# Performance work log

Measured on AMD Instinct MI355X. Metric: run time of the kernel, lower is better.

The kernel has to match this reference:

```python
import jax, jax.numpy as jnp
import numpy as np

B, T, C = 4, 2048, 1024
NH = 16
HD = C // NH


def setup_inputs() -> dict:
    key = jax.random.key(0)
    ks = jax.random.split(key, 5)
    s = 1.0 / np.sqrt(C)
    return {
        "x": jax.random.normal(ks[0], (B, T, C), dtype=jnp.float32),
        "W_qkv": jax.random.normal(ks[1], (C, 3 * C), dtype=jnp.float32) * s,
        "b_qkv": jnp.zeros((3 * C,), dtype=jnp.float32),
        "W_out": jax.random.normal(ks[2], (C, C), dtype=jnp.float32) * s,
        "b_out": jnp.zeros((C,), dtype=jnp.float32),
    }


def reference(x, W_qkv, b_qkv, W_out, b_out):
    Bx, Tx, Cx = x.shape
    qkv = x @ W_qkv + b_qkv                      # [B,T,3C]
    q, k, v = jnp.split(qkv, 3, axis=2)
    # [B,T,C] -> [B,NH,T,HD]
    q = q.reshape(Bx, Tx, NH, HD).transpose(0, 2, 1, 3)
    k = k.reshape(Bx, Tx, NH, HD).transpose(0, 2, 1, 3)
    v = v.reshape(Bx, Tx, NH, HD).transpose(0, 2, 1, 3)
    scale = 1.0 / np.sqrt(HD).astype(np.float32)
    attn = jnp.einsum('bhqd,bhkd->bhqk', q, k) * scale  # [B,NH,T,T]
    causal = jnp.tril(jnp.ones((Tx, Tx), dtype=bool))
    attn = jnp.where(causal[None, None], attn, jnp.float32(-jnp.inf))
    attn = jax.nn.softmax(attn, axis=-1)
    out = jnp.einsum('bhqk,bhkd->bhqd', attn, v)        # [B,NH,T,HD]
    out = out.transpose(0, 2, 1, 3).reshape(Bx, Tx, Cx)
    y = out @ W_out + b_out
    return (y, k, v)
```

## Files before the change

kernel.cpp:

```cpp
#include <hip/hip_runtime.h>
#include <cstdint>
#include <cstddef>

typedef __bf16 bf16x8 __attribute__((ext_vector_type(8)));
typedef __bf16 bf16x4 __attribute__((ext_vector_type(4)));
typedef float  f32x4  __attribute__((ext_vector_type(4)));

#define MFMA16(a, b, c) __builtin_amdgcn_mfma_f32_16x16x32_bf16((a), (b), (c), 0, 0, 0)

#define GLL16(gsrc, ldst)                                                              \
  __builtin_amdgcn_global_load_lds((__attribute__((address_space(1))) void*)(gsrc),    \
                                   (__attribute__((address_space(3))) void*)(ldst),    \
                                   16, 0, 0)

#define QSCALE 0.1803368801111204f


__global__ __launch_bounds__(256)
void cvt_f32_bf16(const float* __restrict__ in, __bf16* __restrict__ out, int n4)
{
    int i = blockIdx.x * 256 + threadIdx.x;
    if (i < n4) {
        float4 v = ((const float4*)in)[i];
        bf16x4 o;
        o[0] = (__bf16)v.x; o[1] = (__bf16)v.y; o[2] = (__bf16)v.z; o[3] = (__bf16)v.w;
        ((bf16x4*)out)[i] = o;
    }
}

__global__ __launch_bounds__(256)
void transpose_cvt(const float* __restrict__ in, __bf16* __restrict__ out, int K, int N)
{
    __shared__ __bf16 tile[32][33];
    const int n0 = blockIdx.x * 32, k0 = blockIdx.y * 32;
    const int tx = threadIdx.x, ty = threadIdx.y;
    #pragma unroll
    for (int i = 0; i < 4; ++i)
        tile[ty + i * 8][tx] = (__bf16)in[(size_t)(k0 + ty + i * 8) * N + n0 + tx];
    __syncthreads();
    #pragma unroll
    for (int i = 0; i < 4; ++i)
        out[(size_t)(n0 + ty + i * 8) * K + k0 + tx] = tile[tx][ty + i * 8];
}


__global__ __launch_bounds__(256)
void vtrans(const float* __restrict__ vout, __bf16* __restrict__ vwst)
{
    const int bh = blockIdx.y;
    const int t0 = blockIdx.x * 64;
    const int tid = threadIdx.x;

    __shared__ __bf16 VT[64][68];

    const int tr = tid >> 4;
    const int dc = (tid & 15) * 4;

    float4 vals[4];
    #pragma unroll
    for (int i = 0; i < 4; ++i)
        vals[i] = *(const float4*)&vout[((size_t)bh * 2048 + t0 + tr + 16 * i) * 64 + dc];

    #pragma unroll
    for (int j = 0; j < 4; ++j) {
        bf16x4 pk;
        pk[0] = (__bf16)(&vals[0].x)[j];
        pk[1] = (__bf16)(&vals[1].x)[j];
        pk[2] = (__bf16)(&vals[2].x)[j];
        pk[3] = (__bf16)(&vals[3].x)[j];
        *(bf16x4*)&VT[dc + j][4 * tr] = pk;
    }
    __syncthreads();

    #pragma unroll
    for (int k = 0; k < 2; ++k) {
        const int c = tid + 256 * k;
        const int d = c >> 3, off = (c & 7) * 8;
        bf16x8 v = *(const bf16x8*)&VT[d][off];
        *(bf16x8*)&vwst[((size_t)bh * 64 + d) * 2048 + t0 + off] = v;
    }
}


__global__ __launch_bounds__(512, 2)
void gemm_qkv(const __bf16* __restrict__ A, const __bf16* __restrict__ Bt,
              const float* __restrict__ bias,
              __bf16* __restrict__ qws, float* __restrict__ kout, float* __restrict__ vout,
              __bf16* __restrict__ kws)
{
    constexpr int K = 1024;
    const int m0 = blockIdx.y * 256, n0 = blockIdx.x * 192;
    const int tid = threadIdx.x;
    const int wave = tid >> 6, lane = tid & 63;
    const int quad = lane >> 4, lr = lane & 15;
    const int wm = wave & 1, wn = wave >> 1;
    const int wrow = wm * 128, wcol = wn * 48;

    __shared__ __bf16 As[2][2][256][32];
    __shared__ __bf16 Bs[2][2][192][32];

    f32x4 acc[8][3];
    #pragma unroll
    for (int mi = 0; mi < 8; ++mi)
      #pragma unroll
      for (int ni = 0; ni < 3; ++ni)
        #pragma unroll
        for (int c = 0; c < 4; ++c) acc[mi][ni][c] = 0.f;

    const __bf16* gA[4];
    #pragma unroll
    for (int l = 0; l < 4; ++l) {
        const int u = tid + 512 * l;
        const int kc = u >> 10;
        const int row = (u >> 2) & 255;
        const int cg = ((u & 3) ^ ((u >> 3) & 3)) * 8;
        gA[l] = A + (size_t)(m0 + row) * K + kc * 32 + cg;
    }
    const __bf16* gB[3];
    #pragma unroll
    for (int l = 0; l < 3; ++l) {
        const int u = tid + 512 * l;
        const int kc = (u >= 768);
        const int row = (u - kc * 768) >> 2;
        const int cg = ((u & 3) ^ ((u >> 3) & 3)) * 8;
        gB[l] = Bt + (size_t)(n0 + row) * K + kc * 32 + cg;
    }
    char* lA = (char*)As + tid * 16;
    char* lB = (char*)Bs + tid * 16;

    const int sw = (quad ^ ((lr >> 1) & 3)) * 8;

    GLL16(gA[0], lA);
    GLL16(gA[1], lA + 8192);
    GLL16(gA[2], lA + 16384);
    GLL16(gA[3], lA + 24576);
    GLL16(gB[0], lB);
    GLL16(gB[1], lB + 8192);
    GLL16(gB[2], lB + 16384);
    GLL16(gA[0] + 64, lA + 32768);
    GLL16(gA[1] + 64, lA + 40960);
    asm volatile("s_waitcnt vmcnt(2)" ::: "memory");
    asm volatile("s_barrier" ::: "memory");

    bf16x8 bfv[3];

#define PHASE(buf, kc, mh, ...)                                                    \
    do {                                                                           \
        if ((mh) == 0) {                                                           \
            bfv[0] = *(const bf16x8*)&Bs[buf][kc][wcol      + lr][sw];             \
            bfv[1] = *(const bf16x8*)&Bs[buf][kc][wcol + 16 + lr][sw];             \
            bfv[2] = *(const bf16x8*)&Bs[buf][kc][wcol + 32 + lr][sw];             \
        }                                                                          \
        bf16x8 af0 = *(const bf16x8*)&As[buf][kc][wrow + (mh)*64      + lr][sw];   \
        bf16x8 af1 = *(const bf16x8*)&As[buf][kc][wrow + (mh)*64 + 16 + lr][sw];   \
        bf16x8 af2 = *(const bf16x8*)&As[buf][kc][wrow + (mh)*64 + 32 + lr][sw];   \
        bf16x8 af3 = *(const bf16x8*)&As[buf][kc][wrow + (mh)*64 + 48 + lr][sw];   \
        __VA_ARGS__                                                                \
        asm volatile("s_barrier" ::: "memory");                                    \
        __builtin_amdgcn_s_setprio(1);                                             \
        acc[(mh)*4+0][0] = MFMA16(af0, bfv[0], acc[(mh)*4+0][0]);                  \
        acc[(mh)*4+0][1] = MFMA16(af0, bfv[1], acc[(mh)*4+0][1]);                  \
        acc[(mh)*4+0][2] = MFMA16(af0, bfv[2], acc[(mh)*4+0][2]);                  \
        acc[(mh)*4+1][0] = MFMA16(af1, bfv[0], acc[(mh)*4+1][0]);                  \
        acc[(mh)*4+1][1] = MFMA16(af1, bfv[1], acc[(mh)*4+1][1]);                  \
        acc[(mh)*4+1][2] = MFMA16(af1, bfv[2], acc[(mh)*4+1][2]);                  \
        acc[(mh)*4+2][0] = MFMA16(af2, bfv[0], acc[(mh)*4+2][0]);                  \
        acc[(mh)*4+2][1] = MFMA16(af2, bfv[1], acc[(mh)*4+2][1]);                  \
        acc[(mh)*4+2][2] = MFMA16(af2, bfv[2], acc[(mh)*4+2][2]);                  \
        acc[(mh)*4+3][0] = MFMA16(af3, bfv[0], acc[(mh)*4+3][0]);                  \
        acc[(mh)*4+3][1] = MFMA16(af3, bfv[1], acc[(mh)*4+3][1]);                  \
        acc[(mh)*4+3][2] = MFMA16(af3, bfv[2], acc[(mh)*4+3][2]);                  \
        __builtin_amdgcn_s_setprio(0);                                             \
        asm volatile("s_barrier" ::: "memory");                                    \
    } while (0)

    for (int it = 0; it < 8; ++it) {
        const bool more = (it < 7);

        PHASE(0, 0, 0, {
            GLL16(gA[2] + 64, lA + 16384 + 32768);
            GLL16(gA[3] + 64, lA + 24576 + 32768);
            GLL16(gB[0] + 64, lB + 24576);
            GLL16(gB[1] + 64, lB +  8192 + 24576);
            GLL16(gB[2] + 64, lB + 16384 + 24576);
        });
        PHASE(0, 0, 1, {});
        PHASE(0, 1, 0, {
            if (more) { GLL16(gA[0] + 128, lA); GLL16(gA[1] + 128, lA + 8192); }
        });
        PHASE(0, 1, 1, {
            if (more) asm volatile("s_waitcnt vmcnt(2)" ::: "memory");
            else      asm volatile("s_waitcnt vmcnt(0)" ::: "memory");
        });
        PHASE(1, 0, 0, {
            if (more) {
                GLL16(gA[2] + 128, lA + 16384);
                GLL16(gA[3] + 128, lA + 24576);
                GLL16(gB[0] + 128, lB);
                GLL16(gB[1] + 128, lB + 8192);
                GLL16(gB[2] + 128, lB + 16384);
            }
        });
        PHASE(1, 0, 1, {});
        PHASE(1, 1, 0, {
            if (more) { GLL16(gA[0] + 192, lA + 32768); GLL16(gA[1] + 192, lA + 40960); }
        });
        PHASE(1, 1, 1, {
            if (more) asm volatile("s_waitcnt vmcnt(2)" ::: "memory");
            else      asm volatile("s_waitcnt vmcnt(0)" ::: "memory");
        });

        #pragma unroll
        for (int l = 0; l < 4; ++l) gA[l] += 128;
        #pragma unroll
        for (int l = 0; l < 3; ++l) gB[l] += 128;
    }
#undef PHASE

    #pragma unroll
    for (int ni = 0; ni < 3; ++ni) {
        const int gn = n0 + wcol + ni * 16 + lr;
        const float bv = bias[gn];
        const int sec = gn >> 10;
        const int cn = gn & 1023, hh = cn >> 6, dd = cn & 63;
        #pragma unroll
        for (int mi = 0; mi < 8; ++mi) {
            const int gm0 = m0 + wrow + mi * 16 + quad * 4;
            const int b = gm0 >> 11, t0 = gm0 & 2047;
            const size_t tb = ((size_t)b * 16 + hh) * 2048;
            if (sec == 0) {
                #pragma unroll
                for (int r = 0; r < 4; ++r)
                    qws[(tb + t0 + r) * 64 + dd] = (__bf16)((acc[mi][ni][r] + bv) * QSCALE);
            } else if (sec == 1) {
                #pragma unroll
                for (int r = 0; r < 4; ++r) {
                    const float val = acc[mi][ni][r] + bv;
                    kout[(tb + t0 + r) * 64 + dd] = val;
                    kws [(tb + t0 + r) * 64 + dd] = (__bf16)val;
                }
            } else {
                #pragma unroll
                for (int r = 0; r < 4; ++r)
                    vout[(tb + t0 + r) * 64 + dd] = acc[mi][ni][r] + bv;
            }
        }
    }
}


__global__ __launch_bounds__(256)
void gemm_out(const __bf16* __restrict__ A, const __bf16* __restrict__ Bt,
              const float* __restrict__ bias, float* __restrict__ y)
{
    constexpr int K = 1024;
    const int m0 = blockIdx.y * 64, n0 = blockIdx.x * 128;
    const int tid = threadIdx.x;
    const int wave = tid >> 6, lane = tid & 63;
    const int quad = lane >> 4, lr = lane & 15;
    const int wrow = (wave & 1) * 32, wcol = (wave >> 1) * 64;

    __shared__ __bf16 As[64 * 32];
    __shared__ __bf16 Bs[128 * 32];

    f32x4 acc[2][4];
    #pragma unroll
    for (int mi = 0; mi < 2; ++mi)
      #pragma unroll
      for (int ni = 0; ni < 4; ++ni)
        #pragma unroll
        for (int c = 0; c < 4; ++c) acc[mi][ni][c] = 0.f;

    const int ua = tid, u0 = tid, u1 = tid + 256;
    const int cga = ((ua & 3) ^ ((ua >> 3) & 3)) * 8;
    const int cg0 = ((u0 & 3) ^ ((u0 >> 3) & 3)) * 8;
    const int cg1 = ((u1 & 3) ^ ((u1 >> 3) & 3)) * 8;
    const __bf16* ga  = A  + (size_t)(m0 + (ua >> 2)) * K + cga;
    const __bf16* gb0 = Bt + (size_t)(n0 + (u0 >> 2)) * K + cg0;
    const __bf16* gb1 = Bt + (size_t)(n0 + (u1 >> 2)) * K + cg1;
    __bf16* la  = As + ua * 8;
    __bf16* lb0 = Bs + u0 * 8;
    __bf16* lb1 = Bs + u1 * 8;

    const int sw = (quad ^ ((lr >> 1) & 3)) * 8;

    for (int kt = 0; kt < K; kt += 32) {
        __syncthreads();
        GLL16(ga + kt, la);
        GLL16(gb0 + kt, lb0);
        GLL16(gb1 + kt, lb1);
        __syncthreads();
        bf16x8 af[2], bfv[4];
        #pragma unroll
        for (int mi = 0; mi < 2; ++mi)
            af[mi] = *(const bf16x8*)&As[(wrow + mi * 16 + lr) * 32 + sw];
        #pragma unroll
        for (int ni = 0; ni < 4; ++ni)
            bfv[ni] = *(const bf16x8*)&Bs[(wcol + ni * 16 + lr) * 32 + sw];
        #pragma unroll
        for (int mi = 0; mi < 2; ++mi)
          #pragma unroll
          for (int ni = 0; ni < 4; ++ni)
            acc[mi][ni] = MFMA16(af[mi], bfv[ni], acc[mi][ni]);
    }

    #pragma unroll
    for (int ni = 0; ni < 4; ++ni) {
        const int gn = n0 + wcol + ni * 16 + lr;
        const float bv = bias[gn];
        #pragma unroll
        for (int mi = 0; mi < 2; ++mi) {
            #pragma unroll
            for (int r = 0; r < 4; ++r) {
                const int gm = m0 + wrow + mi * 16 + quad * 4 + r;
                y[(size_t)gm * 1024 + gn] = acc[mi][ni][r] + bv;
            }
        }
    }
}


__global__ __launch_bounds__(256, 2)
void attn_fused(const __bf16* __restrict__ qws, const __bf16* __restrict__ kws,
                const __bf16* __restrict__ vwst, __bf16* __restrict__ attnws)
{
    const int bh = blockIdx.x;
    const int tid = threadIdx.x;
    const int wave = tid >> 6, lane = tid & 63;
    const int quad = lane >> 4, lr = lane & 15;

    const int jqp[2] = { (int)blockIdx.y, 15 - (int)blockIdx.y };
    const int ntp[2] = { 2 * (jqp[0] + 1), 2 * (jqp[1] + 1) };
    const int nt0 = ntp[0];
    const int ntot = 34;

    __shared__ __bf16 Ks [3][2][64][32];
    __shared__ __bf16 Vts[3][2][64][32];
    __shared__ __bf16 Ps [4][32][72];

    const int srow = tid >> 2;
    const int scg  = ((tid & 3) ^ ((tid >> 3) & 3)) * 8;
    const __bf16* kb = kws  + ((size_t)bh * 2048 + srow) * 64 + scg;
    const __bf16* vb = vwst + ((size_t)bh * 64 + srow) * 2048 + scg;
    char* lk = (char*)Ks  + tid * 16;
    char* lv = (char*)Vts + tid * 16;

    const int sw = (quad ^ ((lr >> 1) & 3)) * 8;

    bf16x8 ones;
    #pragma unroll
    for (int j = 0; j < 8; ++j) ones[j] = (__bf16)1.0f;

    bf16x8 aq[2][2][2];
    #pragma unroll
    for (int h = 0; h < 2; ++h)
      #pragma unroll
      for (int mi = 0; mi < 2; ++mi) {
        const __bf16* qb = qws + ((size_t)bh * 2048 + jqp[h] * 128 + wave * 32 + mi * 16 + lr) * 64 + quad * 8;
        aq[h][mi][0] = *(const bf16x8*)qb;
        aq[h][mi][1] = *(const bf16x8*)(qb + 32);
      }

#define PREFETCH(j, buf)                                                \
    do {                                                                \
        GLL16(kb + (size_t)(j) * 4096,      lk + (buf) * 8192);         \
        GLL16(kb + (size_t)(j) * 4096 + 32, lk + (buf) * 8192 + 4096);  \
        GLL16(vb + (j) * 64,                lv + (buf) * 8192);         \
        GLL16(vb + (j) * 64 + 32,           lv + (buf) * 8192 + 4096);  \
    } while (0)

    PREFETCH(0, 0);
    PREFETCH(1, 1);

    bf16x4 oreg[2][2][4];

    int pos = 0;
    for (int h = 0; h < 2; ++h) {
        const int jq = jqp[h];
        const int NT = ntp[h];

        f32x4 o_acc[2][4], l_acc[2];
        #pragma unroll
        for (int mi = 0; mi < 2; ++mi) {
            #pragma unroll
            for (int r = 0; r < 4; ++r) l_acc[mi][r] = 0.f;
            #pragma unroll
            for (int n = 0; n < 4; ++n)
                #pragma unroll
                for (int r = 0; r < 4; ++r) o_acc[mi][n][r] = 0.f;
        }

        for (int jt = 0; jt < NT; ++jt, ++pos) {
            const int cur = pos % 3;
            if (pos + 1 < ntot) {
                asm volatile("s_waitcnt vmcnt(4)" ::: "memory");
            } else {
                asm volatile("s_waitcnt vmcnt(0)" ::: "memory");
            }
            asm volatile("s_waitcnt lgkmcnt(0)" ::: "memory");
            asm volatile("s_barrier" ::: "memory");
            if (pos + 2 < ntot) {
                const int p2 = pos + 2;
                const int nj = (p2 < nt0) ? p2 : p2 - nt0;
                PREFETCH(nj, p2 % 3);
            }

            const bool lastTile = (jt == NT - 1);
            if (!(lastTile && wave < 2)) {
                bf16x8 bk[4][2];
                #pragma unroll
                for (int ni = 0; ni < 4; ++ni) {
                    bk[ni][0] = *(const bf16x8*)&Ks[cur][0][ni * 16 + lr][sw];
                    bk[ni][1] = *(const bf16x8*)&Ks[cur][1][ni * 16 + lr][sw];
                }
                f32x4 sacc[2][4];
                #pragma unroll
                for (int mi = 0; mi < 2; ++mi)
                  #pragma unroll
                  for (int ni = 0; ni < 4; ++ni)
                    #pragma unroll
                    for (int c = 0; c < 4; ++c) sacc[mi][ni][c] = -12.f;
                #pragma unroll
                for (int ni = 0; ni < 4; ++ni)
                  #pragma unroll
                  for (int mi = 0; mi < 2; ++mi) {
                    sacc[mi][ni] = MFMA16(aq[h][mi][0], bk[ni][0], sacc[mi][ni]);
                    sacc[mi][ni] = MFMA16(aq[h][mi][1], bk[ni][1], sacc[mi][ni]);
                  }

                const bool needMask = (jt == NT - 2 && wave < 2) || (lastTile && wave >= 2);
                if (needMask) {
                    const int c0 = jt * 64 + lr;
                    #pragma unroll
                    for (int mi = 0; mi < 2; ++mi) {
                        const int t0 = jq * 128 + wave * 32 + mi * 16 + quad * 4;
                        #pragma unroll
                        for (int ni = 0; ni < 4; ++ni)
                          #pragma unroll
                          for (int r = 0; r < 4; ++r)
                            if (c0 + ni * 16 > t0 + r) sacc[mi][ni][r] = -1e30f;
                    }
                }

                #pragma unroll
                for (int mi = 0; mi < 2; ++mi)
                  #pragma unroll
                  for (int r = 0; r < 4; ++r) {
                    bf16x4 pp;
                    #pragma unroll
                    for (int ni = 0; ni < 4; ++ni)
                        pp[ni] = (__bf16)__builtin_amdgcn_exp2f(sacc[mi][ni][r]);
                    *(bf16x4*)&Ps[wave][mi * 16 + quad * 4 + r][4 * lr] = pp;
                  }

                asm volatile("s_waitcnt lgkmcnt(0)" ::: "memory");

                bf16x8 bv[4][2];
                #pragma unroll
                for (int n = 0; n < 4; ++n) {
                    bv[n][0] = *(const bf16x8*)&Vts[cur][0][n * 16 + lr][sw];
                    bv[n][1] = *(const bf16x8*)&Vts[cur][1][n * 16 + lr][sw];
                }
                #pragma unroll
                for (int mi = 0; mi < 2; ++mi) {
                    bf16x8 ap0 = *(const bf16x8*)&Ps[wave][mi * 16 + lr][quad * 8];
                    bf16x8 ap1 = *(const bf16x8*)&Ps[wave][mi * 16 + lr][32 + quad * 8];
                    l_acc[mi] = MFMA16(ap0, ones, l_acc[mi]);
                    l_acc[mi] = MFMA16(ap1, ones, l_acc[mi]);
                    #pragma unroll
                    for (int n = 0; n < 4; ++n) {
                        o_acc[mi][n] = MFMA16(ap0, bv[n][0], o_acc[mi][n]);
                        o_acc[mi][n] = MFMA16(ap1, bv[n][1], o_acc[mi][n]);
                    }
                }
            }
        }

        #pragma unroll
        for (int mi = 0; mi < 2; ++mi)
          #pragma unroll
          for (int r = 0; r < 4; ++r) {
            const float inv = 1.f / l_acc[mi][r];
            #pragma unroll
            for (int n = 0; n < 4; ++n)
                oreg[h][mi][n][r] = (__bf16)(o_acc[mi][n][r] * inv);
          }
    }

    const int b = bh >> 4, h16 = bh & 15;
    #pragma unroll
    for (int h = 0; h < 2; ++h)
      #pragma unroll
      for (int mi = 0; mi < 2; ++mi)
        #pragma unroll
        for (int r = 0; r < 4; ++r) {
            const int t = jqp[h] * 128 + wave * 32 + mi * 16 + quad * 4 + r;
            #pragma unroll
            for (int n = 0; n < 4; ++n)
                attnws[(((size_t)b * 2048 + t) * 16 + h16) * 64 + n * 16 + lr] =
                    oreg[h][mi][n][r];
        }
#undef PREFETCH
}


extern "C" void kernel_launch(void* const* d_in, const int* in_sizes, int n_in,
                              void* d_out, int out_size, void* d_ws, size_t ws_size,
                              hipStream_t stream)
{
    (void)in_sizes; (void)n_in; (void)out_size; (void)ws_size;

    const float* x    = (const float*)d_in[0];
    const float* Wqkv = (const float*)d_in[1];
    const float* bqkv = (const float*)d_in[2];
    const float* Wout = (const float*)d_in[3];
    const float* bout = (const float*)d_in[4];

    float* y    = (float*)d_out;
    float* kout = y + 8388608;
    float* vout = kout + 8388608;

    char* ws = (char*)d_ws;
    __bf16* xb    = (__bf16*)(ws);
    __bf16* wqkvt = (__bf16*)(ws + (16u << 20));
    __bf16* woutt = (__bf16*)(ws + (22u << 20));
    __bf16* qws   = (__bf16*)(ws + (24u << 20));
    __bf16* kws   = (__bf16*)(ws + (40u << 20));
    __bf16* vwst  = (__bf16*)(ws + (56u << 20));
    __bf16* attnw = (__bf16*)(ws + (72u << 20));

    cvt_f32_bf16<<<8192, 256, 0, stream>>>(x, xb, 2097152);
    transpose_cvt<<<dim3(96, 32), dim3(32, 8), 0, stream>>>(Wqkv, wqkvt, 1024, 3072);
    transpose_cvt<<<dim3(32, 32), dim3(32, 8), 0, stream>>>(Wout, woutt, 1024, 1024);
    gemm_qkv<<<dim3(16, 32), 512, 0, stream>>>(xb, wqkvt, bqkv, qws, kout, vout, kws);
    vtrans<<<dim3(32, 64), 256, 0, stream>>>(vout, vwst);
    attn_fused<<<dim3(64, 8), 256, 0, stream>>>(qws, kws, vwst, attnw);
    gemm_out<<<dim3(8, 128), 256, 0, stream>>>(attnw, woutt, bout, y);
}
```

Baseline: 304.5 us.

## Double-buffer LDS fragment registers to overlap ds_reads with MFMAs in QKV GEMM

Restructures the QKV GEMM main loop so A and B fragments for the next half-step are loaded from LDS into a second register set while the current set feeds the MFMAs. It also removes most of the per-phase barriers, keeping only those needed around buffer reuse and global-to-LDS waits. The goal is to hide LDS read latency and cut barrier stalls. The cost is extra VGPRs from the doubled fragment registers, which could hurt the 2-blocks-per-CU occupancy target, plus subtler synchronisation correctness.

```diff
diff --git a/kernel.cpp b/kernel.cpp
--- a/kernel.cpp
+++ b/kernel.cpp
@@ -93,8 +93,7 @@
     const int tid = threadIdx.x;
     const int wave = tid >> 6, lane = tid & 63;
     const int quad = lane >> 4, lr = lane & 15;
-    const int wm = wave & 1, wn = wave >> 1;
-    const int wrow = wm * 128, wcol = wn * 48;
+    const int wrow = (wave & 1) * 128, wcol = (wave >> 1) * 48;
 
     __shared__ __bf16 As[2][2][256][32];
     __shared__ __bf16 Bs[2][2][192][32];
@@ -129,6 +128,43 @@
     char* lB = (char*)Bs + tid * 16;
 
     const int sw = (quad ^ ((lr >> 1) & 3)) * 8;
+
+#define BARF  asm volatile("s_barrier" ::: "memory")
+#define WAITV2 asm volatile("s_waitcnt vmcnt(2)" ::: "memory")
+#define WAITV0 asm volatile("s_waitcnt vmcnt(0)" ::: "memory")
+
+#define LDB(bf, buf, kc)                                                   \
+    do {                                                                   \
+        bf[0] = *(const bf16x8*)&Bs[buf][kc][wcol      + lr][sw];          \
+        bf[1] = *(const bf16x8*)&Bs[buf][kc][wcol + 16 + lr][sw];          \
+        bf[2] = *(const bf16x8*)&Bs[buf][kc][wcol + 32 + lr][sw];          \
+    } while (0)
+
+#define LDA(af, buf, kc, mh)                                                  \
+    do {                                                                      \
+        af[0] = *(const bf16x8*)&As[buf][kc][wrow + (mh)*64      + lr][sw];   \
+        af[1] = *(const bf16x8*)&As[buf][kc][wrow + (mh)*64 + 16 + lr][sw];   \
+        af[2] = *(const bf16x8*)&As[buf][kc][wrow + (mh)*64 + 32 + lr][sw];   \
+        af[3] = *(const bf16x8*)&As[buf][kc][wrow + (mh)*64 + 48 + lr][sw];   \
+    } while (0)
+
+#define FMA12(af, bf, mh)                                                  \
+    do {                                                                   \
+        __builtin_amdgcn_s_setprio(1);                                     \
+        acc[(mh)*4+0][0] = MFMA16(af[0], bf[0], acc[(mh)*4+0][0]);         \
+        acc[(mh)*4+0][1] = MFMA16(af[0], bf[1], acc[(mh)*4+0][1]);         \
+        acc[(mh)*4+0][2] = MFMA16(af[0], bf[2], acc[(mh)*4+0][2]);         \
+        acc[(mh)*4+1][0] = MFMA16(af[1], bf[0], acc[(mh)*4+1][0]);         \
+        acc[(mh)*4+1][1] = MFMA16(af[1], bf[1], acc[(mh)*4+1][1]);         \
+        acc[(mh)*4+1][2] = MFMA16(af[1], bf[2], acc[(mh)*4+1][2]);         \
+        acc[(mh)*4+2][0] = MFMA16(af[2], bf[0], acc[(mh)*4+2][0]);         \
+        acc[(mh)*4+2][1] = MFMA16(af[2], bf[1], acc[(mh)*4+2][1]);         \
+        acc[(mh)*4+2][2] = MFMA16(af[2], bf[2], acc[(mh)*4+2][2]);         \
+        acc[(mh)*4+3][0] = MFMA16(af[3], bf[0], acc[(mh)*4+3][0]);         \
+        acc[(mh)*4+3][1] = MFMA16(af[3], bf[1], acc[(mh)*4+3][1]);         \
+        acc[(mh)*4+3][2] = MFMA16(af[3], bf[2], acc[(mh)*4+3][2]);         \
+        __builtin_amdgcn_s_setprio(0);                                     \
+    } while (0)
 
     GLL16(gA[0], lA);
     GLL16(gA[1], lA + 8192);
@@ -139,83 +175,78 @@
     GLL16(gB[2], lB + 16384);
     GLL16(gA[0] + 64, lA + 32768);
     GLL16(gA[1] + 64, lA + 40960);
-    asm volatile("s_waitcnt vmcnt(2)" ::: "memory");
-    asm volatile("s_barrier" ::: "memory");
-
-    bf16x8 bfv[3];
-
-#define PHASE(buf, kc, mh, ...)                                                    \
-    do {                                                                           \
-        if ((mh) == 0) {                                                           \
-            bfv[0] = *(const bf16x8*)&Bs[buf][kc][wcol      + lr][sw];             \
-            bfv[1] = *(const bf16x8*)&Bs[buf][kc][wcol + 16 + lr][sw];             \
-            bfv[2] = *(const bf16x8*)&Bs[buf][kc][wcol + 32 + lr][sw];             \
-        }                                                                          \
-        bf16x8 af0 = *(const bf16x8*)&As[buf][kc][wrow + (mh)*64      + lr][sw];   \
-        bf16x8 af1 = *(const bf16x8*)&As[buf][kc][wrow + (mh)*64 + 16 + lr][sw];   \
-        bf16x8 af2 = *(const bf16x8*)&As[buf][kc][wrow + (mh)*64 + 32 + lr][sw];   \
-        bf16x8 af3 = *(const bf16x8*)&As[buf][kc][wrow + (mh)*64 + 48 + lr][sw];   \
-        __VA_ARGS__                                                                \
-        asm volatile("s_barrier" ::: "memory");                                    \
-        __builtin_amdgcn_s_setprio(1);                                             \
-        acc[(mh)*4+0][0] = MFMA16(af0, bfv[0], acc[(mh)*4+0][0]);                  \
-        acc[(mh)*4+0][1] = MFMA16(af0, bfv[1], acc[(mh)*4+0][1]);                  \
-        acc[(mh)*4+0][2] = MFMA16(af0, bfv[2], acc[(mh)*4+0][2]);                  \
-        acc[(mh)*4+1][0] = MFMA16(af1, bfv[0], acc[(mh)*4+1][0]);                  \
-        acc[(mh)*4+1][1] = MFMA16(af1, bfv[1], acc[(mh)*4+1][1]);                  \
-        acc[(mh)*4+1][2] = MFMA16(af1, bfv[2], acc[(mh)*4+1][2]);                  \
-        acc[(mh)*4+2][0] = MFMA16(af2, bfv[0], acc[(mh)*4+2][0]);                  \
-        acc[(mh)*4+2][1] = MFMA16(af2, bfv[1], acc[(mh)*4+2][1]);                  \
-        acc[(mh)*4+2][2] = MFMA16(af2, bfv[2], acc[(mh)*4+2][2]);                  \
-        acc[(mh)*4+3][0] = MFMA16(af3, bfv[0], acc[(mh)*4+3][0]);                  \
-        acc[(mh)*4+3][1] = MFMA16(af3, bfv[1], acc[(mh)*4+3][1]);                  \
-        acc[(mh)*4+3][2] = MFMA16(af3, bfv[2], acc[(mh)*4+3][2]);                  \
-        __builtin_amdgcn_s_setprio(0);                                             \
-        asm volatile("s_barrier" ::: "memory");                                    \
-    } while (0)
+    WAITV2;
+    BARF;
+
+    bf16x8 afA[4], afB[4], bfA[3], bfB[3];
+    LDB(bfA, 0, 0);
+    LDA(afA, 0, 0, 0);
 
     for (int it = 0; it < 8; ++it) {
         const bool more = (it < 7);
 
-        PHASE(0, 0, 0, {
-            GLL16(gA[2] + 64, lA + 16384 + 32768);
-            GLL16(gA[3] + 64, lA + 24576 + 32768);
-            GLL16(gB[0] + 64, lB + 24576);
-            GLL16(gB[1] + 64, lB +  8192 + 24576);
-            GLL16(gB[2] + 64, lB + 16384 + 24576);
-        });
-        PHASE(0, 0, 1, {});
-        PHASE(0, 1, 0, {
-            if (more) { GLL16(gA[0] + 128, lA); GLL16(gA[1] + 128, lA + 8192); }
-        });
-        PHASE(0, 1, 1, {
-            if (more) asm volatile("s_waitcnt vmcnt(2)" ::: "memory");
-            else      asm volatile("s_waitcnt vmcnt(0)" ::: "memory");
-        });
-        PHASE(1, 0, 0, {
-            if (more) {
-                GLL16(gA[2] + 128, lA + 16384);
-                GLL16(gA[3] + 128, lA + 24576);
-                GLL16(gB[0] + 128, lB);
-                GLL16(gB[1] + 128, lB + 8192);
-                GLL16(gB[2] + 128, lB + 16384);
-            }
-        });
-        PHASE(1, 0, 1, {});
-        PHASE(1, 1, 0, {
-            if (more) { GLL16(gA[0] + 192, lA + 32768); GLL16(gA[1] + 192, lA + 40960); }
-        });
-        PHASE(1, 1, 1, {
-            if (more) asm volatile("s_waitcnt vmcnt(2)" ::: "memory");
-            else      asm volatile("s_waitcnt vmcnt(0)" ::: "memory");
-        });
+        GLL16(gA[2] + 64, lA + 49152);
+        GLL16(gA[3] + 64, lA + 57344);
+        GLL16(gB[0] + 64, lB + 24576);
+        GLL16(gB[1] + 64, lB + 32768);
+        GLL16(gB[2] + 64, lB + 40960);
+        LDA(afB, 0, 0, 1);
+        FMA12(afA, bfA, 0);
+
+        LDA(afA, 0, 1, 0);
+        LDB(bfB, 0, 1);
+        FMA12(afB, bfA, 1);
+        BARF;
+
+        if (more) { GLL16(gA[0] + 128, lA); GLL16(gA[1] + 128, lA + 8192); }
+        LDA(afB, 0, 1, 1);
+        FMA12(afA, bfB, 0);
+
+        if (more) WAITV2; else WAITV0;
+        BARF;
+        LDA(afA, 1, 0, 0);
+        LDB(bfA, 1, 0);
+        FMA12(afB, bfB, 1);
+        BARF;
+
+        if (more) {
+            GLL16(gA[2] + 128, lA + 16384);
+            GLL16(gA[3] + 128, lA + 24576);
+            GLL16(gB[0] + 128, lB);
+            GLL16(gB[1] + 128, lB + 8192);
+            GLL16(gB[2] + 128, lB + 16384);
+        }
+        LDA(afB, 1, 0, 1);
+        FMA12(afA, bfA, 0);
+
+        LDA(afA, 1, 1, 0);
+        LDB(bfB, 1, 1);
+        FMA12(afB, bfA, 1);
+        BARF;
+
+        if (more) { GLL16(gA[0] + 192, lA + 32768); GLL16(gA[1] + 192, lA + 40960); }
+        LDA(afB, 1, 1, 1);
+        FMA12(afA, bfB, 0);
+
+        if (more) WAITV2; else WAITV0;
+        BARF;
+        LDA(afA, 0, 0, 0);
+        LDB(bfA, 0, 0);
+        FMA12(afB, bfB, 1);
+        BARF;
 
         #pragma unroll
         for (int l = 0; l < 4; ++l) gA[l] += 128;
         #pragma unroll
         for (int l = 0; l < 3; ++l) gB[l] += 128;
     }
-#undef PHASE
+
+#undef FMA12
+#undef LDA
+#undef LDB
+#undef BARF
+#undef WAITV2
+#undef WAITV0
 
     #pragma unroll
     for (int ni = 0; ni < 3; ++ni) {
```

Measured after the change: 306.6 us. Within noise of the previous version (+0.7%).
